# Kernel tuning notes

Hardware: AMD Instinct MI355X
Metric: run time of the kernel (lower is better)

## Reference

```python
import jax, jax.numpy as jnp
import numpy as np
from jax import lax

BATCH = 8192
HID = 10
IN = 64
STEPS = 512
REVERSE = True


def setup_inputs() -> dict:
    key = jax.random.key(0)
    ks = jax.random.split(key, 9)
    s_in = 1.0 / np.sqrt(HID)
    return {
        "hidden": jax.random.normal(ks[0], (1, BATCH, HID), dtype=jnp.float32),
        "w_ih": jax.random.uniform(ks[1], (3 * HID, IN), jnp.float32, -s_in, s_in),
        "w_hh": jax.random.uniform(ks[2], (3 * HID, HID), jnp.float32, -s_in, s_in),
        "b_ih": jax.random.uniform(ks[3], (3 * HID,), jnp.float32, -s_in, s_in),
        "b_hh": jax.random.uniform(ks[4], (3 * HID,), jnp.float32, -s_in, s_in),
        "l1_w": jax.random.uniform(ks[5], (10, HID), jnp.float32, -s_in, s_in),
        "l1_b": jax.random.uniform(ks[6], (10,), jnp.float32, -s_in, s_in),
        "l2_w": jax.random.uniform(ks[7], (IN, 10), jnp.float32, -s_in, s_in),
        "l2_b": jax.random.uniform(ks[8], (IN,), jnp.float32, -s_in, s_in),
        "step": STEPS,
    }


def _gru_cell(h, x, w_ih, w_hh, b_ih, b_hh):
    # PyTorch GRU gate order: reset, update, new
    gi = x @ w_ih.T + b_ih  # [B, 3H]
    gh = h @ w_hh.T + b_hh  # [B, 3H]
    i_r, i_z, i_n = jnp.split(gi, 3, axis=-1)
    h_r, h_z, h_n = jnp.split(gh, 3, axis=-1)
    r = jax.nn.sigmoid(i_r + h_r)
    z = jax.nn.sigmoid(i_z + h_z)
    n = jnp.tanh(i_n + r * h_n)
    return (1.0 - z) * n + z * h


def reference(hidden, w_ih, w_hh, b_ih, b_hh, l1_w, l1_b, l2_w, l2_b, step):
    h0 = hidden[0]  # [B, H]
    B = h0.shape[0]
    x0 = jnp.zeros((B, IN), dtype=h0.dtype)  # first GRU input is zeros

    def body(carry, _):
        h, x = carry
        h_new = _gru_cell(h, x, w_ih, w_hh, b_ih, b_hh)
        o = h_new @ l1_w.T + l1_b          # l1 on GRU output
        x_next = o @ l2_w.T + l2_b         # l2 feeds next GRU step
        return (h_new, x_next), o

    _, outs = lax.scan(body, (h0, x0), None, length=step)  # [T, B, 10]
    outs = jnp.transpose(outs, (1, 0, 2))  # [B, T, 10]
    if REVERSE:
        outs = outs[:, ::-1, :]
    return outs
```

## Files before the change

kernel.cpp:

```cpp
#include <hip/hip_runtime.h>

#define HID 10
#define STEPS 512

typedef __attribute__((ext_vector_type(2))) float v2f;

template<int F>
static __device__ __forceinline__ float swz(float v) {
    return __int_as_float(__builtin_amdgcn_ds_swizzle(__float_as_int(v), (F << 5) | 0x10));
}

static __device__ __forceinline__ v2f pk_mul(v2f a, v2f b) {
    v2f d;
    asm("v_pk_mul_f32 %0, %1, %2" : "=v"(d) : "v"(a), "v"(b));
    return d;
}
static __device__ __forceinline__ void pk_fma(v2f& acc, v2f a, v2f b) {
    asm("v_pk_fma_f32 %0, %1, %2, %0" : "+v"(acc) : "v"(a), "v"(b));
}

__global__ __launch_bounds__(64, 2) void gru_decoder_kernel(
    const float* __restrict__ hidden, const float* __restrict__ w_ih,
    const float* __restrict__ w_hh, const float* __restrict__ b_ih,
    const float* __restrict__ b_hh, const float* __restrict__ l1_w,
    const float* __restrict__ l1_b, const float* __restrict__ l2_w,
    const float* __restrict__ l2_b, float* __restrict__ out)
{
    __shared__ float sWx[640];
    __shared__ float sbx[64];
    __shared__ float sWgi[300];
    __shared__ float sbgi[30];
    __shared__ float sWhh[300];
    __shared__ alignas(16) float sstage[4 * 168];

    const int lane = threadIdx.x;
    const int f    = lane & 15;
    const int grp  = lane >> 4;
    const int b    = blockIdx.x * 4 + grp;
    const bool ok  = (f < HID);
    const int fi   = ok ? f : 0;

    for (int e = lane; e < 640; e += 64) {
        int i = e / 10, j = e - i * 10;
        float acc = 0.f;
        #pragma unroll
        for (int k = 0; k < 10; ++k) acc += l2_w[i * 10 + k] * l1_w[k * 10 + j];
        sWx[e] = acc;
    }
    {
        float acc = l2_b[lane];
        #pragma unroll
        for (int k = 0; k < 10; ++k) acc += l2_w[lane * 10 + k] * l1_b[k];
        sbx[lane] = acc;
    }
    for (int e = lane; e < 300; e += 64) sWhh[e] = w_hh[e];
    __syncthreads();
    for (int e = lane; e < 300; e += 64) {
        int m = e / 10, j = e - m * 10;
        float acc = 0.f;
        for (int k = 0; k < 64; ++k) acc += w_ih[m * 64 + k] * sWx[k * 10 + j];
        sWgi[e] = acc;
    }
    if (lane < 30) {
        float acc = b_ih[lane];
        for (int k = 0; k < 64; ++k) acc += w_ih[lane * 64 + k] * sbx[k];
        sbgi[lane] = acc;
    }
    __syncthreads();

    const float LOG2E = 1.4426950408889634f;
    const float S2    = 2.f * LOG2E;

    v2f wr2[5], wz2[5], wni2[5], wnh2[5], wo2[5];
    #pragma unroll
    for (int i = 0; i < 5; ++i) {
        int k0 = 2 * i, k1 = 2 * i + 1;
        if (ok) {
            wr2[i]  = (v2f){-(sWgi[fi * 10 + k0] + sWhh[fi * 10 + k0]) * LOG2E,
                            -(sWgi[fi * 10 + k1] + sWhh[fi * 10 + k1]) * LOG2E};
            wz2[i]  = (v2f){-(sWgi[(10 + fi) * 10 + k0] + sWhh[(10 + fi) * 10 + k0]) * LOG2E,
                            -(sWgi[(10 + fi) * 10 + k1] + sWhh[(10 + fi) * 10 + k1]) * LOG2E};
            wni2[i] = (v2f){sWgi[(20 + fi) * 10 + k0] * S2, sWgi[(20 + fi) * 10 + k1] * S2};
            wnh2[i] = (v2f){sWhh[(20 + fi) * 10 + k0] * S2, sWhh[(20 + fi) * 10 + k1] * S2};
            wo2[i]  = (v2f){l1_w[fi * 10 + k0], l1_w[fi * 10 + k1]};
        } else {
            v2f zz = {0.f, 0.f};
            wr2[i] = zz; wz2[i] = zz; wni2[i] = zz; wnh2[i] = zz; wo2[i] = zz;
        }
    }
    const float br  = ok ? -(sbgi[fi] + b_hh[fi]) * LOG2E : 0.f;
    const float bz  = ok ? -(sbgi[10 + fi] + b_hh[10 + fi]) * LOG2E : 0.f;
    const float bni = ok ? sbgi[20 + fi] * S2 : 0.f;
    const float bnh = ok ? b_hh[20 + fi] * S2 : 0.f;
    const float bo  = ok ? l1_b[fi] : 0.f;
    const float br0  = ok ? -(b_ih[fi] + b_hh[fi]) * LOG2E : 0.f;
    const float bz0  = ok ? -(b_ih[10 + fi] + b_hh[10 + fi]) * LOG2E : 0.f;
    const float bni0 = ok ? b_ih[20 + fi] * S2 : 0.f;

    float h = ok ? hidden[(size_t)b * HID + f] : 0.f;

    v2f h2[5];
    #define GATHER()                                             \
        h2[0] = (v2f){swz<0>(h), swz<1>(h)};                     \
        h2[1] = (v2f){swz<2>(h), swz<3>(h)};                     \
        h2[2] = (v2f){swz<4>(h), swz<5>(h)};                     \
        h2[3] = (v2f){swz<6>(h), swz<7>(h)};                     \
        h2[4] = (v2f){swz<8>(h), swz<9>(h)};

    GATHER();

    float* wp = ok ? &sstage[grp * 168 + 150 + f] : &sstage[grp * 168 + 166];
    const int vdec = ok ? 10 : 0;
    const int vinc = vdec * 16;
    float* pf = out + (size_t)b * (STEPS * HID) + (size_t)(STEPS - 16) * HID + 2 * f;
    const int rb = grp * 168 + 2 * f;

    #define O_WRITE()                                            \
        {                                                        \
            v2f ao = pk_mul(wo2[0], h2[0]);                      \
            pk_fma(ao, wo2[1], h2[1]);                           \
            pk_fma(ao, wo2[2], h2[2]);                           \
            pk_fma(ao, wo2[3], h2[3]);                           \
            pk_fma(ao, wo2[4], h2[4]);                           \
            *wp = ao.x + ao.y + bo;                              \
            wp -= vdec;                                          \
        }

    {
        float ha[10];
        #pragma unroll
        for (int i = 0; i < 5; ++i) { ha[2 * i] = h2[i].x; ha[2 * i + 1] = h2[i].y; }
        float pr = 0.f, pz = 0.f, ph = 0.f;
        #pragma unroll
        for (int k = 0; k < 10; ++k) {
            pr += sWhh[fi * 10 + k] * ha[k];
            pz += sWhh[(10 + fi) * 10 + k] * ha[k];
            ph += sWhh[(20 + fi) * 10 + k] * ha[k];
        }
        float vr = br0 - pr * LOG2E;
        float vz = bz0 - pz * LOG2E;
        float r = __builtin_amdgcn_rcpf(1.f + __builtin_amdgcn_exp2f(vr));
        float z = __builtin_amdgcn_rcpf(1.f + __builtin_amdgcn_exp2f(vz));
        float y = bni0 + r * (ph * S2 + bnh);
        float n = 1.f - 2.f * __builtin_amdgcn_rcpf(1.f + __builtin_amdgcn_exp2f(y));
        h = ok ? (n + z * (h - n)) : 0.f;
        GATHER();
        O_WRITE();
    }

    #pragma unroll 1
    for (int t = 1; t < STEPS; ++t) {
        v2f ar = pk_mul(wr2[0], h2[0]);
        v2f az = pk_mul(wz2[0], h2[0]);
        v2f ai = pk_mul(wni2[0], h2[0]);
        v2f ah = pk_mul(wnh2[0], h2[0]);
        #pragma unroll
        for (int i = 1; i < 5; ++i) {
            pk_fma(ar, wr2[i], h2[i]);
            pk_fma(az, wz2[i], h2[i]);
            pk_fma(ai, wni2[i], h2[i]);
            pk_fma(ah, wnh2[i], h2[i]);
        }
        float vr = (ar.x + ar.y) + br;
        float vz = (az.x + az.y) + bz;
        float r = __builtin_amdgcn_rcpf(1.f + __builtin_amdgcn_exp2f(vr));
        float z = __builtin_amdgcn_rcpf(1.f + __builtin_amdgcn_exp2f(vz));
        float y = ((ai.x + ai.y) + bni) + r * ((ah.x + ah.y) + bnh);
        float n = 1.f - 2.f * __builtin_amdgcn_rcpf(1.f + __builtin_amdgcn_exp2f(y));
        h = n + z * (h - n);
        GATHER();
        O_WRITE();

        if ((t & 15) == 15) {
            #pragma unroll
            for (int c = 0; c < 5; ++c) {
                v2f v = *reinterpret_cast<const v2f*>(&sstage[rb + 32 * c]);
                __builtin_nontemporal_store(v, reinterpret_cast<v2f*>(pf + 32 * c));
            }
            pf -= 16 * HID;
            wp += vinc;
        }
    }
}

extern "C" void kernel_launch(void* const* d_in, const int* in_sizes, int n_in,
                              void* d_out, int out_size, void* d_ws, size_t ws_size,
                              hipStream_t stream) {
    (void)in_sizes; (void)n_in; (void)d_ws; (void)ws_size; (void)out_size;
    dim3 grid(2048), block(64);
    gru_decoder_kernel<<<grid, block, 0, stream>>>(
        (const float*)d_in[0], (const float*)d_in[1], (const float*)d_in[2],
        (const float*)d_in[3], (const float*)d_in[4], (const float*)d_in[5],
        (const float*)d_in[6], (const float*)d_in[7], (const float*)d_in[8],
        (float*)d_out);
}
```

Baseline: 330.4 us.

## Replace ds_swizzle with DPP row broadcast and write outputs directly

Broadcasts each hidden element within a 16-lane row using DPP row_newbcast instead of ds_swizzle, which keeps the per-step gather off the LDS pipe. Drops the shared-memory staging buffer and its 16-step batched nontemporal stores in favour of one direct global store per step per valid lane. Also unrolls the recurrence loop by two. This shortens the serial dependency chain per step, at the cost of many more small scattered global stores instead of coalesced 8-byte bursts.

```diff
diff --git a/kernel.cpp b/kernel.cpp
--- a/kernel.cpp
+++ b/kernel.cpp
@@ -6,8 +6,9 @@
 typedef __attribute__((ext_vector_type(2))) float v2f;
 
 template<int F>
-static __device__ __forceinline__ float swz(float v) {
-    return __int_as_float(__builtin_amdgcn_ds_swizzle(__float_as_int(v), (F << 5) | 0x10));
+static __device__ __forceinline__ float rowbc(float v) {
+    int s = __float_as_int(v);
+    return __int_as_float(__builtin_amdgcn_update_dpp(s, s, 0x150 | F, 0xF, 0xF, false));
 }
 
 static __device__ __forceinline__ v2f pk_mul(v2f a, v2f b) {
@@ -31,12 +32,10 @@
     __shared__ float sWgi[300];
     __shared__ float sbgi[30];
     __shared__ float sWhh[300];
-    __shared__ alignas(16) float sstage[4 * 168];
 
     const int lane = threadIdx.x;
     const int f    = lane & 15;
-    const int grp  = lane >> 4;
-    const int b    = blockIdx.x * 4 + grp;
+    const int b    = blockIdx.x * 4 + (lane >> 4);
     const bool ok  = (f < HID);
     const int fi   = ok ? f : 0;
 
@@ -101,30 +100,15 @@
 
     v2f h2[5];
     #define GATHER()                                             \
-        h2[0] = (v2f){swz<0>(h), swz<1>(h)};                     \
-        h2[1] = (v2f){swz<2>(h), swz<3>(h)};                     \
-        h2[2] = (v2f){swz<4>(h), swz<5>(h)};                     \
-        h2[3] = (v2f){swz<6>(h), swz<7>(h)};                     \
-        h2[4] = (v2f){swz<8>(h), swz<9>(h)};
+        h2[0] = (v2f){rowbc<0>(h), rowbc<1>(h)};                 \
+        h2[1] = (v2f){rowbc<2>(h), rowbc<3>(h)};                 \
+        h2[2] = (v2f){rowbc<4>(h), rowbc<5>(h)};                 \
+        h2[3] = (v2f){rowbc<6>(h), rowbc<7>(h)};                 \
+        h2[4] = (v2f){rowbc<8>(h), rowbc<9>(h)};
 
     GATHER();
 
-    float* wp = ok ? &sstage[grp * 168 + 150 + f] : &sstage[grp * 168 + 166];
-    const int vdec = ok ? 10 : 0;
-    const int vinc = vdec * 16;
-    float* pf = out + (size_t)b * (STEPS * HID) + (size_t)(STEPS - 16) * HID + 2 * f;
-    const int rb = grp * 168 + 2 * f;
-
-    #define O_WRITE()                                            \
-        {                                                        \
-            v2f ao = pk_mul(wo2[0], h2[0]);                      \
-            pk_fma(ao, wo2[1], h2[1]);                           \
-            pk_fma(ao, wo2[2], h2[2]);                           \
-            pk_fma(ao, wo2[3], h2[3]);                           \
-            pk_fma(ao, wo2[4], h2[4]);                           \
-            *wp = ao.x + ao.y + bo;                              \
-            wp -= vdec;                                          \
-        }
+    float* pb = out + (size_t)b * (STEPS * HID) + (size_t)(STEPS - 1) * HID + f;
 
     {
         float ha[10];
@@ -145,11 +129,20 @@
         float n = 1.f - 2.f * __builtin_amdgcn_rcpf(1.f + __builtin_amdgcn_exp2f(y));
         h = ok ? (n + z * (h - n)) : 0.f;
         GATHER();
-        O_WRITE();
+        float o = bo;
+        {
+            v2f ao = pk_mul(wo2[0], h2[0]);
+            pk_fma(ao, wo2[1], h2[1]);
+            pk_fma(ao, wo2[2], h2[2]);
+            pk_fma(ao, wo2[3], h2[3]);
+            pk_fma(ao, wo2[4], h2[4]);
+            o += ao.x + ao.y;
+        }
+        if (ok) pb[0] = o;
+        pb -= HID;
     }
 
-    #pragma unroll 1
-    for (int t = 1; t < STEPS; ++t) {
+    auto STEP = [&]() {
         v2f ar = pk_mul(wr2[0], h2[0]);
         v2f az = pk_mul(wz2[0], h2[0]);
         v2f ai = pk_mul(wni2[0], h2[0]);
@@ -169,18 +162,22 @@
         float n = 1.f - 2.f * __builtin_amdgcn_rcpf(1.f + __builtin_amdgcn_exp2f(y));
         h = n + z * (h - n);
         GATHER();
-        O_WRITE();
+        v2f ao = pk_mul(wo2[0], h2[0]);
+        pk_fma(ao, wo2[1], h2[1]);
+        pk_fma(ao, wo2[2], h2[2]);
+        pk_fma(ao, wo2[3], h2[3]);
+        pk_fma(ao, wo2[4], h2[4]);
+        float o = (ao.x + ao.y) + bo;
+        if (ok) pb[0] = o;
+        pb -= HID;
+    };
 
-        if ((t & 15) == 15) {
-            #pragma unroll
-            for (int c = 0; c < 5; ++c) {
-                v2f v = *reinterpret_cast<const v2f*>(&sstage[rb + 32 * c]);
-                __builtin_nontemporal_store(v, reinterpret_cast<v2f*>(pf + 32 * c));
-            }
-            pf -= 16 * HID;
-            wp += vinc;
-        }
+    #pragma unroll 1
+    for (int tp = 0; tp < 255; ++tp) {
+        STEP();
+        STEP();
     }
+    STEP();
 }
 
 extern "C" void kernel_launch(void* const* d_in, const int* in_sizes, int n_in,
```

New measurement: 331.4 us. About the same (+0.3%).
